# Kernel optimization log

Measured on AMD Instinct MI355X. Metric: run time of the kernel, lower is better.

Reference implementation:

```python
import jax, jax.numpy as jnp
import numpy as np
import math

HEAD_DIM = 128
N_HEADS = 32
N_KV_HEADS = 8
HIDDEN = 4096
ROPE_BASE = 10000.0


def _rope_cos_sin(position_ids):
    # inv_freq: [D/2]
    inv_freq = 1.0 / (ROPE_BASE ** (jnp.arange(0, HEAD_DIM, 2, dtype=jnp.float32) / HEAD_DIM))
    freqs = position_ids.astype(jnp.float32)[..., None] * inv_freq  # [B,S,D/2]
    emb = jnp.concatenate([freqs, freqs], axis=-1)  # [B,S,D]
    return jnp.cos(emb), jnp.sin(emb)


def _rotate_half(x):
    x1, x2 = jnp.split(x, 2, axis=-1)
    return jnp.concatenate([-x2, x1], axis=-1)


def setup_inputs() -> dict:
    key = jax.random.key(0)
    ks = jax.random.split(key, 5)
    B, S = 1, 2048
    inp = {
        "hidden_states": jax.random.normal(ks[0], (B, S, HIDDEN), dtype=jnp.float32),
        "position_ids": jnp.arange(B * S, dtype=jnp.int32).reshape(B, S),
        "Wq": jax.random.normal(ks[1], (HIDDEN, N_HEADS * HEAD_DIM), dtype=jnp.float32) * 0.02,
        "Wk": jax.random.normal(ks[2], (HIDDEN, N_KV_HEADS * HEAD_DIM), dtype=jnp.float32) * 0.02,
        "Wv": jax.random.normal(ks[3], (HIDDEN, N_KV_HEADS * HEAD_DIM), dtype=jnp.float32) * 0.02,
        "Wo": jax.random.normal(ks[4], (N_HEADS * HEAD_DIM, HIDDEN), dtype=jnp.float32) * 0.02,
    }
    return inp


def reference(hidden_states, position_ids, Wq, Wk, Wv, Wo):
    B, S, _ = hidden_states.shape
    G = N_HEADS // N_KV_HEADS

    q = (hidden_states @ Wq).reshape(B, S, N_HEADS, HEAD_DIM).transpose(0, 2, 1, 3)      # [B,H,S,D]
    k = (hidden_states @ Wk).reshape(B, S, N_KV_HEADS, HEAD_DIM).transpose(0, 2, 1, 3)   # [B,Hkv,S,D]
    v = (hidden_states @ Wv).reshape(B, S, N_KV_HEADS, HEAD_DIM).transpose(0, 2, 1, 3)

    cos, sin = _rope_cos_sin(position_ids)          # [B,S,D]
    cos = cos[:, None, :, :]                         # [B,1,S,D]
    sin = sin[:, None, :, :]
    q = q * cos + _rotate_half(q) * sin
    k = k * cos + _rotate_half(k) * sin

    # GQA head expansion (repeat_interleave over head dim)
    k = jnp.repeat(k, G, axis=1)                     # [B,H,S,D]
    v = jnp.repeat(v, G, axis=1)

    scale = 1.0 / math.sqrt(HEAD_DIM)
    scores = jnp.einsum("bhqd,bhkd->bhqk", q, k) * scale  # [B,H,S,S]
    causal = jnp.triu(jnp.full((S, S), -jnp.inf, dtype=scores.dtype), k=1)
    scores = scores + causal[None, None]
    probs = jax.nn.softmax(scores.astype(jnp.float32), axis=-1).astype(q.dtype)
    ctx = jnp.einsum("bhqk,bhkd->bhqd", probs, v)    # [B,H,S,D]
    ctx = ctx.transpose(0, 2, 1, 3).reshape(B, S, N_HEADS * HEAD_DIM)
    return ctx @ Wo
```

## Files before the change

kernel.cpp:

```cpp
#include <hip/hip_runtime.h>
#include <hip/hip_bf16.h>
#include <math.h>

#define SEQ 2048
#define NHEADS 32
#define NKVH 8
#define HD 128
#define HIDDEN 4096
#define NQKV 6144

typedef unsigned short u16;
typedef unsigned int u32;
typedef __attribute__((ext_vector_type(8))) __bf16 bf16x8;
typedef __attribute__((ext_vector_type(4))) float f32x4;
typedef __attribute__((ext_vector_type(4))) u16 u16x4;
typedef __attribute__((ext_vector_type(4))) u32 u32x4;

__device__ __forceinline__ u16 f2bf(float f) {
  u32 u = __builtin_bit_cast(u32, f);
  u32 r = (u + 0x7fffu + ((u >> 16) & 1u)) >> 16;
  return (u16)r;
}
__device__ __forceinline__ float bf2f(u16 h) {
  return __builtin_bit_cast(float, ((u32)h) << 16);
}
__device__ __forceinline__ void gload_lds16(const void* g, void* l) {
  __builtin_amdgcn_global_load_lds(
      (const __attribute__((address_space(1))) u32*)g,
      (__attribute__((address_space(3))) u32*)l, 16, 0, 0);
}

#define BAR __builtin_amdgcn_s_barrier()
#define PRIO1 __builtin_amdgcn_s_setprio(1)
#define PRIO0 __builtin_amdgcn_s_setprio(0)
#define VMW(n) asm volatile("s_waitcnt vmcnt(" #n ")" ::: "memory")

__global__ void __launch_bounds__(256) prep_all(
    const float* __restrict__ hs, u16* __restrict__ Xb,
    const float* __restrict__ Wq, u16* __restrict__ Wqt,
    const float* __restrict__ Wk, u16* __restrict__ Wkt,
    const float* __restrict__ Wv, u16* __restrict__ Wvt) {
  const int bid = blockIdx.x;
  if (bid < 8192) {
    const int i = (bid * 256 + threadIdx.x) * 4;
    const float4 v = *(const float4*)(hs + i);
    u16x4 o;
    o.x = f2bf(v.x); o.y = f2bf(v.y); o.z = f2bf(v.z); o.w = f2bf(v.w);
    *(u16x4*)(Xb + i) = o;
    return;
  }
  __shared__ float tile[64][65];
  const float* src; u16* dst; int C, lc, tb;
  const int b2 = bid - 8192;
  if (b2 < 4096) { src = Wq; dst = Wqt; C = 4096; lc = 6; tb = b2; }
  else if (b2 < 5120) { src = Wk; dst = Wkt; C = 1024; lc = 4; tb = b2 - 4096; }
  else { src = Wv; dst = Wvt; C = 1024; lc = 4; tb = b2 - 5120; }
  const int r0 = (tb >> lc) * 64, c0 = (tb & ((1 << lc) - 1)) * 64;
  const int tx = threadIdx.x & 63, ty = threadIdx.x >> 6;
#pragma unroll
  for (int j = 0; j < 16; ++j)
    tile[ty + j * 4][tx] = src[(size_t)(r0 + ty + j * 4) * C + c0 + tx];
  __syncthreads();
#pragma unroll
  for (int j = 0; j < 16; ++j)
    dst[(size_t)(c0 + ty + j * 4) * 4096 + r0 + tx] = f2bf(tile[tx][ty + j * 4]);
}

__global__ void __launch_bounds__(256) post_qkv(u16* __restrict__ qkv, u16* __restrict__ vtb,
                                                const int* __restrict__ pos) {
  const int bid = blockIdx.x;
  if (bid < 20480) {
    int idx, hoff, sshift;
    float oscale;
    if (bid < 16384) {
      idx = bid * 256 + threadIdx.x;
      hoff = ((idx >> 6) & 31) * 128;
      sshift = 11;
      oscale = 0.08838834764831845f * 1.44269504088896340f;
    } else {
      idx = (bid - 16384) * 256 + threadIdx.x;
      hoff = 4096 + ((idx >> 6) & 7) * 128;
      sshift = 9;
      oscale = 1.0f;
    }
    const int j = idx & 63;
    const int s = idx >> sshift;
    if (s >= SEQ) return;
    const float p = (float)pos[s];
    const float invf = __expf((float)j * -0.14391156831212787f);
    const float ang = p * invf;
    const float c = cosf(ang), sn = sinf(ang);
    u16* bp = qkv + (size_t)s * NQKV + hoff + j;
    const float x1 = bf2f(bp[0]), x2 = bf2f(bp[64]);
    bp[0] = f2bf((x1 * c - x2 * sn) * oscale);
    bp[64] = f2bf((x2 * c + x1 * sn) * oscale);
    return;
  }
  __shared__ u16 tile[32][34];
  const int b2 = bid - 20480;
  const int c0 = (b2 & 31) * 32, r0 = (b2 >> 5) * 32;
  const int tx = threadIdx.x & 31, ty = threadIdx.x >> 5;
#pragma unroll
  for (int i = 0; i < 4; ++i)
    tile[ty + i * 8][tx] = qkv[(size_t)(r0 + ty + i * 8) * NQKV + 5120 + c0 + tx];
  __syncthreads();
#pragma unroll
  for (int i = 0; i < 4; ++i)
    vtb[(size_t)(c0 + ty + i * 8) * 2048 + r0 + tx] = tile[tx][ty + i * 8];
}

__global__ void __launch_bounds__(512) gemm_qkv(
    const u16* __restrict__ A, const u16* __restrict__ B, u16* __restrict__ C) {
  __shared__ u16 As[2][256 * 64];
  __shared__ u16 Bs[2][192 * 64];
  const int t = threadIdx.x;
  const int lane = t & 63, w = t >> 6;
  const int wr = w >> 2, wc = w & 3;
  const int l15 = lane & 15, l4 = lane >> 4;

  const int bid = blockIdx.x;
  const int xcd = bid & 7, ii = bid >> 3;
  const int byt = xcd, bxt = ii;
  const int row0 = byt * 256, col0 = bxt * 192;

  auto stageA_part = [&](int buf, int tile, int gfirst) {
#pragma unroll
    for (int gg = 0; gg < 2; ++gg) {
      const int g = gfirst + gg * 2;
      const int o = (g * 512 + t) * 16;
      const int ridx = o >> 7;
      const int slot = (o >> 4) & 7;
      gload_lds16(A + (size_t)(row0 + ridx) * 4096 + (tile << 6) + ((slot ^ (ridx & 7)) << 3),
                  (char*)&As[buf][0] + o);
    }
  };
  auto stageB = [&](int buf, int tile) {
#pragma unroll
    for (int g = 0; g < 3; ++g) {
      const int o = (g * 512 + t) * 16;
      const int ridx = o >> 7;
      const int slot = (o >> 4) & 7;
      gload_lds16(B + (size_t)(col0 + ridx) * 4096 + (tile << 6) + ((slot ^ (ridx & 7)) << 3),
                  (char*)&Bs[buf][0] + o);
    }
  };

  bf16x8 af[4][2], bfr[3][2];
  auto loadA = [&](int buf, int mh) {
#pragma unroll
    for (int f = 0; f < 4; ++f)
#pragma unroll
      for (int ks = 0; ks < 2; ++ks) {
        const int idx2 = wr * 128 + mh * 64 + f * 16 + l15;
        const int slot = ks * 4 + l4;
        af[f][ks] = *(const bf16x8*)((const char*)&As[buf][0] + idx2 * 128 +
                                     ((slot ^ (idx2 & 7)) << 4));
      }
  };
  auto loadB = [&](int buf) {
#pragma unroll
    for (int e = 0; e < 3; ++e)
#pragma unroll
      for (int ks = 0; ks < 2; ++ks) {
        const int idx2 = wc * 48 + e * 16 + l15;
        const int slot = ks * 4 + l4;
        bfr[e][ks] = *(const bf16x8*)((const char*)&Bs[buf][0] + idx2 * 128 +
                                      ((slot ^ (idx2 & 7)) << 4));
      }
  };

  f32x4 acc0[4][3], acc1[4][3];
#pragma unroll
  for (int f = 0; f < 4; ++f)
#pragma unroll
    for (int e = 0; e < 3; ++e) {
      acc0[f][e] = f32x4{0.f, 0.f, 0.f, 0.f};
      acc1[f][e] = f32x4{0.f, 0.f, 0.f, 0.f};
    }

  const int nkt = 4096 >> 6;

  stageA_part(0, 0, 0); stageA_part(0, 0, 1); stageB(0, 0);
  stageA_part(1, 1, 0); stageA_part(1, 1, 1); stageB(1, 1);
  VMW(7);
  BAR;

  for (int kt = 0; kt < nkt; ++kt) {
    const int buf = kt & 1;
    loadA(buf, 0); loadB(buf);
    if (kt >= 1 && kt + 1 < nkt) { stageA_part(buf ^ 1, kt + 1, 1); stageB(buf ^ 1, kt + 1); }
    BAR;
    PRIO1;
#pragma unroll
    for (int f = 0; f < 4; ++f)
#pragma unroll
      for (int e = 0; e < 3; ++e)
#pragma unroll
        for (int ks = 0; ks < 2; ++ks)
          acc0[f][e] = __builtin_amdgcn_mfma_f32_16x16x32_bf16(af[f][ks], bfr[e][ks], acc0[f][e],
                                                               0, 0, 0);
    PRIO0;
    BAR;
    loadA(buf, 1);
    if (kt + 2 < nkt) stageA_part(buf, kt + 2, 0);
    BAR;
    PRIO1;
#pragma unroll
    for (int f = 0; f < 4; ++f)
#pragma unroll
      for (int e = 0; e < 3; ++e)
#pragma unroll
        for (int ks = 0; ks < 2; ++ks)
          acc1[f][e] = __builtin_amdgcn_mfma_f32_16x16x32_bf16(af[f][ks], bfr[e][ks], acc1[f][e],
                                                               0, 0, 0);
    PRIO0;
    if (kt + 2 < nkt) { VMW(2); } else { VMW(0); }
    BAR;
  }

#pragma unroll
  for (int f = 0; f < 4; ++f)
#pragma unroll
    for (int e = 0; e < 3; ++e) {
      const int colb = col0 + wc * 48 + e * 16 + l15;
      const int r0a = row0 + wr * 128 + f * 16 + l4 * 4;
#pragma unroll
      for (int r = 0; r < 4; ++r)
        C[(size_t)(r0a + r) * NQKV + colb] = f2bf(acc0[f][e][r]);
      const int r0b = r0a + 64;
#pragma unroll
      for (int r = 0; r < 4; ++r)
        C[(size_t)(r0b + r) * NQKV + colb] = f2bf(acc1[f][e][r]);
    }
}

template <int MH, int NH>
__device__ __forceinline__ void mfq16(f32x4 (&acc)[4][4], const bf16x8 (&af)[2][2],
                                      const bf16x8 (&b)[2][2]) {
#pragma unroll
  for (int f = 0; f < 2; ++f)
#pragma unroll
    for (int e = 0; e < 2; ++e)
#pragma unroll
      for (int ks = 0; ks < 2; ++ks)
        acc[MH * 2 + f][NH * 2 + e] = __builtin_amdgcn_mfma_f32_16x16x32_bf16(
            af[f][ks], b[e][ks], acc[MH * 2 + f][NH * 2 + e], 0, 0, 0);
}

__global__ void __launch_bounds__(512, 2) gemm8p16(
    const u16* __restrict__ A, const u16* __restrict__ B, float* __restrict__ C) {
  __shared__ u16 As[2][2][64 * 64];
  __shared__ u16 Bs[2][2][128 * 64];
  const int t = threadIdx.x;
  const int lane = t & 63, w = t >> 6;
  const int wr = w >> 2, wc = w & 3;
  const int l15 = lane & 15, l4 = lane >> 4;

  const int flat = blockIdx.x;
  const int xcd = flat & 7, idx = flat >> 3;
  const int bxt = idx & 15, byt = xcd * 2 + (idx >> 4);
  const int row0 = byt * 128, col0 = bxt * 256;

  auto stageA = [&](int buf, int half, int tile) {
    const int o = t * 16;
    const int ridx = o >> 7;
    const int slot = (o >> 4) & 7;
    const int gr = (ridx >> 5) * 64 + half * 32 + (ridx & 31);
    gload_lds16(A + (size_t)(row0 + gr) * 4096 + (tile << 6) + ((slot ^ (ridx & 7)) << 3),
                (char*)&As[buf][half][0] + o);
  };
  auto stageB = [&](int buf, int half, int tile) {
#pragma unroll
    for (int g = 0; g < 2; ++g) {
      const int o = (g * 512 + t) * 16;
      const int ridx = o >> 7;
      const int slot = (o >> 4) & 7;
      const int gn = (ridx >> 5) * 64 + half * 32 + (ridx & 31);
      gload_lds16(B + (size_t)(col0 + gn) * 4096 + (tile << 6) + ((slot ^ (ridx & 7)) << 3),
                  (char*)&Bs[buf][half][0] + o);
    }
  };

  bf16x8 af[2][2], bf0[2][2], bf1[2][2];
  auto loadA = [&](int buf, int half) {
#pragma unroll
    for (int f = 0; f < 2; ++f)
#pragma unroll
      for (int ks = 0; ks < 2; ++ks) {
        const int idx2 = wr * 32 + f * 16 + l15;
        const int slot = ks * 4 + l4;
        af[f][ks] = *(const bf16x8*)((const char*)&As[buf][half][0] + idx2 * 128 +
                                     ((slot ^ (idx2 & 7)) << 4));
      }
  };
  auto loadB = [&](int buf, int half, bf16x8 (&dst)[2][2]) {
#pragma unroll
    for (int e = 0; e < 2; ++e)
#pragma unroll
      for (int ks = 0; ks < 2; ++ks) {
        const int idx2 = wc * 32 + e * 16 + l15;
        const int slot = ks * 4 + l4;
        dst[e][ks] = *(const bf16x8*)((const char*)&Bs[buf][half][0] + idx2 * 128 +
                                      ((slot ^ (idx2 & 7)) << 4));
      }
  };

  f32x4 acc[4][4];
#pragma unroll
  for (int m_ = 0; m_ < 4; ++m_)
#pragma unroll
    for (int n_ = 0; n_ < 4; ++n_) acc[m_][n_] = f32x4{0.f, 0.f, 0.f, 0.f};

  const int nit = (4096 >> 6) >> 1;

  stageA(0, 0, 0); stageB(0, 0, 0); stageB(0, 1, 0); stageA(0, 1, 0);
  stageA(1, 0, 1); stageB(1, 0, 1); stageB(1, 1, 1); stageA(1, 1, 1);
  VMW(6);
  BAR;

  for (int i = 0; i < nit; ++i) {
    const int tb = 2 * i;
    const bool g2 = (i + 1 < nit);
    loadA(0, 0); loadB(0, 0, bf0);
    BAR; PRIO1; mfq16<0, 0>(acc, af, bf0); PRIO0; BAR;
    loadB(0, 1, bf1);
    if (g2) { stageA(0, 0, tb + 2); stageB(0, 0, tb + 2); }
    BAR; PRIO1; mfq16<0, 1>(acc, af, bf1); PRIO0; BAR;
    loadA(0, 1);
    if (g2) stageB(0, 1, tb + 2);
    BAR; PRIO1; mfq16<1, 1>(acc, af, bf1); PRIO0; BAR;
    if (g2) stageA(0, 1, tb + 2);
    BAR; PRIO1; mfq16<1, 0>(acc, af, bf0); PRIO0;
    if (g2) { VMW(6); } else { VMW(0); }
    BAR;
    loadA(1, 0); loadB(1, 0, bf0);
    BAR; PRIO1; mfq16<0, 0>(acc, af, bf0); PRIO0; BAR;
    loadB(1, 1, bf1);
    if (g2) { stageA(1, 0, tb + 3); stageB(1, 0, tb + 3); }
    BAR; PRIO1; mfq16<0, 1>(acc, af, bf1); PRIO0; BAR;
    loadA(1, 1);
    if (g2) stageB(1, 1, tb + 3);
    BAR; PRIO1; mfq16<1, 1>(acc, af, bf1); PRIO0; BAR;
    if (g2) stageA(1, 1, tb + 3);
    BAR; PRIO1; mfq16<1, 0>(acc, af, bf0); PRIO0;
    if (g2) { VMW(6); }
    BAR;
  }

#pragma unroll
  for (int am = 0; am < 4; ++am) {
    const int rowb = row0 + wr * 64 + (am >> 1) * 32 + (am & 1) * 16 + l4 * 4;
#pragma unroll
    for (int an = 0; an < 4; ++an) {
      const int colb = col0 + wc * 64 + (an >> 1) * 32 + (an & 1) * 16 + l15;
#pragma unroll
      for (int r = 0; r < 4; ++r)
        C[(size_t)(rowb + r) * 4096 + colb] = acc[am][an][r];
    }
  }
}

__device__ __forceinline__ void stage_kv512(const u16* __restrict__ qkv, const u16* __restrict__ vt,
                                            const int kvh, const int kv0, u16* KsB, u16* VsB,
                                            const int t) {
#pragma unroll
  for (int i = 0; i < 2; ++i) {
    const int o = (i * 512 + t) * 16;
    const int row = o >> 8;
    const int slot = (o >> 4) & 15;
    gload_lds16(qkv + (size_t)(kv0 + row) * NQKV + 4096 + kvh * HD + ((slot ^ (row & 7)) << 3),
                (char*)KsB + o);
  }
#pragma unroll
  for (int i = 0; i < 2; ++i) {
    const int o = (i * 512 + t) * 16;
    const int row = o >> 7;
    const int slot = (o >> 4) & 7;
    gload_lds16(vt + (size_t)(kvh * HD + row) * SEQ + kv0 + ((slot ^ (row & 7)) << 3),
                (char*)VsB + o);
  }
}

__global__ void __launch_bounds__(512) attn_fwd(const u16* __restrict__ qkv,
                                                const u16* __restrict__ vt, u16* __restrict__ ctx,
                                                const float* __restrict__ Wsrc,
                                                u16* __restrict__ Wdst) {
  __shared__ u16 Ks[2][64 * 128];
  __shared__ u16 Vs[2][128 * 64];
  const int t = threadIdx.x, lane = t & 63, w = t >> 6;
  const int bid = blockIdx.x;

  if (bid >= 512) {
    const int wid = bid - 512;
    float* tf = (float*)&Ks[0][0];
    const int tx = t & 63, ty = t >> 6;
    const int r0 = wid * 64;
    for (int ct = 0; ct < 64; ++ct) {
      const int c0 = ct * 64;
#pragma unroll
      for (int i = 0; i < 8; ++i)
        tf[(ty + i * 8) * 65 + tx] = Wsrc[(size_t)(r0 + ty + i * 8) * 4096 + c0 + tx];
      __syncthreads();
#pragma unroll
      for (int i = 0; i < 8; ++i)
        Wdst[(size_t)(c0 + ty + i * 8) * 4096 + r0 + tx] = f2bf(tf[tx * 65 + ty + i * 8]);
      __syncthreads();
    }
    return;
  }

  const int xcd = bid & 7, bi = bid >> 3;
  const int h = xcd * 4 + (bi & 3);
  const int qbb = 15 - (bi >> 2);
  const int kvh = xcd;
  const int q0 = qbb * 128;
  const int sq_base = q0 + w * 16;
  const int l15 = lane & 15, l4 = lane >> 4;
  const int sq_abs = sq_base + l15;
  const int bw = sq_base >> 6;

  bf16x8 qf[4];
  {
    const u16* qp = qkv + (size_t)sq_abs * NQKV + h * HD + l4 * 8;
#pragma unroll
    for (int kb = 0; kb < 4; ++kb) qf[kb] = *(const bf16x8*)(qp + kb * 32);
  }
  f32x4 po[8];
#pragma unroll
  for (int i = 0; i < 8; ++i) po[i] = f32x4{0.f, 0.f, 0.f, 0.f};
  float mrow = -1e30f;
  float lrow = 0.f;

  const int nb = 2 * qbb + 2;
  stage_kv512(qkv, vt, kvh, 0, Ks[0], Vs[0], t);
  __syncthreads();
  int cur = 0;

  for (int b = 0; b < nb; ++b) {
    if (b + 1 < nb) stage_kv512(qkv, vt, kvh, (b + 1) * 64, Ks[cur ^ 1], Vs[cur ^ 1], t);

    if (b <= bw) {
      f32x4 st[4];
#pragma unroll
      for (int c = 0; c < 4; ++c) st[c] = f32x4{0.f, 0.f, 0.f, 0.f};
#pragma unroll
      for (int c = 0; c < 4; ++c) {
        const int row = c * 16 + l15;
#pragma unroll
        for (int kb = 0; kb < 4; ++kb) {
          const int slot = kb * 4 + l4;
          bf16x8 bk = *(const bf16x8*)((const char*)Ks[cur] + row * 256 + ((slot ^ (row & 7)) << 4));
          st[c] = __builtin_amdgcn_mfma_f32_16x16x32_bf16(bk, qf[kb], st[c], 0, 0, 0);
        }
      }

      if (b == bw) {
#pragma unroll
        for (int c = 0; c < 4; ++c)
#pragma unroll
          for (int r = 0; r < 4; ++r) {
            const int sk = b * 64 + c * 16 + l4 * 4 + r;
            if (sk > sq_abs) st[c][r] = -1e30f;
          }
      }

      float rmax = -3e38f;
#pragma unroll
      for (int c = 0; c < 4; ++c)
        rmax = fmaxf(rmax, fmaxf(fmaxf(st[c][0], st[c][1]), fmaxf(st[c][2], st[c][3])));
      rmax = fmaxf(rmax, __shfl_xor(rmax, 16, 64));
      rmax = fmaxf(rmax, __shfl_xor(rmax, 32, 64));

      const bool skip = __all(rmax <= mrow + 8.f);
      const float mnew = skip ? mrow : fmaxf(mrow, rmax);

      float rs = 0.f;
#pragma unroll
      for (int c = 0; c < 4; ++c) {
        const float e0 = exp2f(st[c][0] - mnew), e1 = exp2f(st[c][1] - mnew);
        const float e2 = exp2f(st[c][2] - mnew), e3 = exp2f(st[c][3] - mnew);
        st[c][0] = e0; st[c][1] = e1; st[c][2] = e2; st[c][3] = e3;
        rs += (e0 + e1) + (e2 + e3);
      }
      rs += __shfl_xor(rs, 16, 64);
      rs += __shfl_xor(rs, 32, 64);

      if (!skip) {
        const float alpha = exp2f(mrow - mnew);
        mrow = mnew;
        lrow = lrow * alpha + rs;
        float av[4];
#pragma unroll
        for (int r = 0; r < 4; ++r) av[r] = __shfl(alpha, l4 * 4 + r, 16);
#pragma unroll
        for (int db = 0; db < 8; ++db)
#pragma unroll
          for (int r = 0; r < 4; ++r) po[db][r] *= av[r];
      } else {
        lrow += rs;
      }

      u32 pk[4][2];
#pragma unroll
      for (int c = 0; c < 4; ++c) {
        pk[c][0] = (u32)f2bf(st[c][0]) | ((u32)f2bf(st[c][1]) << 16);
        pk[c][1] = (u32)f2bf(st[c][2]) | ((u32)f2bf(st[c][3]) << 16);
      }
      const int src01 = l15 + ((lane & 16) << 1);
      const int src23 = src01 + 16;
      const bool lo = (lane & 32) == 0;
#pragma unroll
      for (int kb2 = 0; kb2 < 2; ++kb2) {
        const int c0 = kb2 * 2, c1 = c0 + 1;
        const u32 a0 = (u32)__shfl((int)pk[c0][0], src01, 64);
        const u32 a1 = (u32)__shfl((int)pk[c0][1], src01, 64);
        const u32 a2 = (u32)__shfl((int)pk[c0][0], src23, 64);
        const u32 a3 = (u32)__shfl((int)pk[c0][1], src23, 64);
        const u32 b0 = (u32)__shfl((int)pk[c1][0], src01, 64);
        const u32 b1 = (u32)__shfl((int)pk[c1][1], src01, 64);
        const u32 b2 = (u32)__shfl((int)pk[c1][0], src23, 64);
        const u32 b3 = (u32)__shfl((int)pk[c1][1], src23, 64);
        u32x4 wq;
        wq.x = lo ? a0 : b0;
        wq.y = lo ? a1 : b1;
        wq.z = lo ? a2 : b2;
        wq.w = lo ? a3 : b3;
        const bf16x8 pa = __builtin_bit_cast(bf16x8, wq);
#pragma unroll
        for (int db = 0; db < 8; ++db) {
          const int vrow = db * 16 + l15;
          const int pslot = kb2 * 4 + l4;
          bf16x8 bv =
              *(const bf16x8*)((const char*)Vs[cur] + vrow * 128 + ((pslot ^ (vrow & 7)) << 4));
          po[db] = __builtin_amdgcn_mfma_f32_16x16x32_bf16(pa, bv, po[db], 0, 0, 0);
        }
      }
    }
    __syncthreads();
    cur ^= 1;
  }

  float rl[4];
#pragma unroll
  for (int r = 0; r < 4; ++r) rl[r] = 1.f / __shfl(lrow, l4 * 4 + r, 16);
#pragma unroll
  for (int db = 0; db < 8; ++db)
#pragma unroll
    for (int r = 0; r < 4; ++r) {
      const int sq = sq_base + l4 * 4 + r;
      const int d = db * 16 + l15;
      ctx[(size_t)sq * (NHEADS * HD) + h * HD + d] = f2bf(po[db][r] * rl[r]);
    }
}

extern "C" void kernel_launch(void* const* d_in, const int* in_sizes, int n_in,
                              void* d_out, int out_size, void* d_ws, size_t ws_size,
                              hipStream_t stream) {
  const float* hs = (const float*)d_in[0];
  const int* pos = (const int*)d_in[1];
  const float* Wq = (const float*)d_in[2];
  const float* Wk = (const float*)d_in[3];
  const float* Wv = (const float*)d_in[4];
  const float* Wo = (const float*)d_in[5];

  u16* ws = (u16*)d_ws;
  u16* Xb = ws;
  u16* Wqt = Xb + (size_t)2048 * 4096;
  u16* Wkt = Wqt + (size_t)4096 * 4096;
  u16* Wvt = Wkt + (size_t)1024 * 4096;
  u16* Wot = Wvt + (size_t)1024 * 4096;
  u16* qkvb = Wot + (size_t)4096 * 4096;
  u16* vtb = qkvb + (size_t)2048 * 6144;
  u16* ctx = vtb + (size_t)1024 * 2048;
  const size_t need = ((size_t)(ctx - ws) + (size_t)2048 * 4096) * 2;
  if (ws_size < need) return;

  prep_all<<<14336, 256, 0, stream>>>(hs, Xb, Wq, Wqt, Wk, Wkt, Wv, Wvt);

  gemm_qkv<<<256, 512, 0, stream>>>(Xb, Wqt, qkvb);

  post_qkv<<<22528, 256, 0, stream>>>(qkvb, vtb, pos);

  attn_fwd<<<576, 512, 0, stream>>>(qkvb, vtb, ctx, Wo, Wot);

  gemm8p16<<<256, 512, 0, stream>>>(ctx, Wot, (float*)d_out);
}
```

Before: 330.0 us.

## Move Wo transpose into post_qkv and reorder attention q-block scheduling

```diff
diff --git a/kernel.cpp b/kernel.cpp
--- a/kernel.cpp
+++ b/kernel.cpp
@@ -67,7 +67,9 @@
 }
 
 __global__ void __launch_bounds__(256) post_qkv(u16* __restrict__ qkv, u16* __restrict__ vtb,
-                                                const int* __restrict__ pos) {
+                                                const int* __restrict__ pos,
+                                                const float* __restrict__ Wsrc,
+                                                u16* __restrict__ Wdst) {
   const int bid = blockIdx.x;
   if (bid < 20480) {
     int idx, hoff, sshift;
@@ -96,17 +98,31 @@
     bp[64] = f2bf((x2 * c + x1 * sn) * oscale);
     return;
   }
-  __shared__ u16 tile[32][34];
-  const int b2 = bid - 20480;
-  const int c0 = (b2 & 31) * 32, r0 = (b2 >> 5) * 32;
-  const int tx = threadIdx.x & 31, ty = threadIdx.x >> 5;
-#pragma unroll
-  for (int i = 0; i < 4; ++i)
-    tile[ty + i * 8][tx] = qkv[(size_t)(r0 + ty + i * 8) * NQKV + 5120 + c0 + tx];
+  if (bid < 22528) {
+    __shared__ u16 tile[32][34];
+    const int b2 = bid - 20480;
+    const int c0 = (b2 & 31) * 32, r0 = (b2 >> 5) * 32;
+    const int tx = threadIdx.x & 31, ty = threadIdx.x >> 5;
+#pragma unroll
+    for (int i = 0; i < 4; ++i)
+      tile[ty + i * 8][tx] = qkv[(size_t)(r0 + ty + i * 8) * NQKV + 5120 + c0 + tx];
+    __syncthreads();
+#pragma unroll
+    for (int i = 0; i < 4; ++i)
+      vtb[(size_t)(c0 + ty + i * 8) * 2048 + r0 + tx] = tile[tx][ty + i * 8];
+    return;
+  }
+  __shared__ float tf[64][65];
+  const int tb = bid - 22528;
+  const int r0 = (tb >> 6) * 64, c0 = (tb & 63) * 64;
+  const int tx = threadIdx.x & 63, ty = threadIdx.x >> 6;
+#pragma unroll
+  for (int j = 0; j < 16; ++j)
+    tf[ty + j * 4][tx] = Wsrc[(size_t)(r0 + ty + j * 4) * 4096 + c0 + tx];
   __syncthreads();
 #pragma unroll
-  for (int i = 0; i < 4; ++i)
-    vtb[(size_t)(c0 + ty + i * 8) * 2048 + r0 + tx] = tile[tx][ty + i * 8];
+  for (int j = 0; j < 16; ++j)
+    Wdst[(size_t)(c0 + ty + j * 4) * 4096 + r0 + tx] = f2bf(tf[tx][ty + j * 4]);
 }
 
 __global__ void __launch_bounds__(512) gemm_qkv(
@@ -382,36 +398,15 @@
 }
 
 __global__ void __launch_bounds__(512) attn_fwd(const u16* __restrict__ qkv,
-                                                const u16* __restrict__ vt, u16* __restrict__ ctx,
-                                                const float* __restrict__ Wsrc,
-                                                u16* __restrict__ Wdst) {
+                                                const u16* __restrict__ vt, u16* __restrict__ ctx) {
   __shared__ u16 Ks[2][64 * 128];
   __shared__ u16 Vs[2][128 * 64];
   const int t = threadIdx.x, lane = t & 63, w = t >> 6;
   const int bid = blockIdx.x;
-
-  if (bid >= 512) {
-    const int wid = bid - 512;
-    float* tf = (float*)&Ks[0][0];
-    const int tx = t & 63, ty = t >> 6;
-    const int r0 = wid * 64;
-    for (int ct = 0; ct < 64; ++ct) {
-      const int c0 = ct * 64;
-#pragma unroll
-      for (int i = 0; i < 8; ++i)
-        tf[(ty + i * 8) * 65 + tx] = Wsrc[(size_t)(r0 + ty + i * 8) * 4096 + c0 + tx];
-      __syncthreads();
-#pragma unroll
-      for (int i = 0; i < 8; ++i)
-        Wdst[(size_t)(c0 + ty + i * 8) * 4096 + r0 + tx] = f2bf(tf[tx * 65 + ty + i * 8]);
-      __syncthreads();
-    }
-    return;
-  }
-
   const int xcd = bid & 7, bi = bid >> 3;
   const int h = xcd * 4 + (bi & 3);
-  const int qbb = 15 - (bi >> 2);
+  const int j = bi >> 2;
+  const int qbb = (j < 8) ? (15 - j) : (j - 8);
   const int kvh = xcd;
   const int q0 = qbb * 128;
   const int sq_base = q0 + w * 16;
@@ -579,9 +574,9 @@
 
   gemm_qkv<<<256, 512, 0, stream>>>(Xb, Wqt, qkvb);
 
-  post_qkv<<<22528, 256, 0, stream>>>(qkvb, vtb, pos);
-
-  attn_fwd<<<576, 512, 0, stream>>>(qkvb, vtb, ctx, Wo, Wot);
+  post_qkv<<<26624, 256, 0, stream>>>(qkvb, vtb, pos, Wo, Wot);
+
+  attn_fwd<<<512, 512, 0, stream>>>(qkvb, vtb, ctx);
 
   gemm8p16<<<256, 512, 0, stream>>>(ctx, Wot, (float*)d_out);
 }
```

After: 317.1 us. 3.9% less time.
